# Kernel tuning notes

Measured on AMD Instinct MI355X. Metric: run time of the kernel, lower is better.

The kernel has to match this reference:

```python
import jax, jax.numpy as jnp
import numpy as np

SCALE = 0.125  # 1/sqrt(head_dim=64)

def setup_inputs() -> dict:
    key = jax.random.key(0)
    kq, kk, kv = jax.random.split(key, 3)
    shape = (8, 16, 1024, 64)  # [batch, heads, seq, head_dim]
    q = jax.random.normal(kq, shape, dtype=jnp.float32)
    k = jax.random.normal(kk, shape, dtype=jnp.float32)
    v = jax.random.normal(kv, shape, dtype=jnp.float32)
    return {"q": q, "k": k, "v": v}

def reference(q, k, v):
    # qk = q @ k^T, scaled; softmax over keys; dropout(p=0) is identity; combine with v
    scores = jnp.einsum("bhqd,bhkd->bhqk", q, k) * SCALE
    attn = jax.nn.softmax(scores, axis=-1)
    out = jnp.einsum("bhqk,bhkd->bhqd", attn, v)
    return out
```

## Files before the change

### kernel.cpp

```cpp
#include <hip/hip_runtime.h>
#include <hip/hip_bf16.h>
#include <math.h>

#define SEQ   1024
#define DH    64
#define KBLK  64
#define NBH   128
#define LDK   72
#define C2    0.1803368801111244f
#define DEFER_THR 44.0f

typedef short bf16x8 __attribute__((ext_vector_type(8)));
typedef float f32x4  __attribute__((ext_vector_type(4)));
typedef unsigned u32x4 __attribute__((ext_vector_type(4)));

__device__ inline unsigned short f2bf_rne(float f) {
    union { float f; unsigned u; } x; x.f = f;
    unsigned u = x.u;
    u += 0x7FFFu + ((u >> 16) & 1u);
    return (unsigned short)(u >> 16);
}
__device__ inline unsigned cvt_pk_bf16(float lo, float hi) {
    unsigned r;
    asm("v_cvt_pk_bf16_f32 %0, %1, %2" : "=v"(r) : "v"(lo), "v"(hi));
    return r;
}
__device__ inline void pl32swap(unsigned &a, unsigned &b) {
    asm("v_permlane32_swap_b32 %0, %1" : "+v"(a), "+v"(b));
}
__device__ inline void pl16swap(unsigned &a, unsigned &b) {
    asm("v_permlane16_swap_b32 %0, %1" : "+v"(a), "+v"(b));
}

__device__ inline float wave_red_add(float x) {
    x += __shfl_xor(x, 16);
    x += __shfl_xor(x, 32);
    return x;
}
__device__ inline float wave_red_max(float x) {
    x = fmaxf(x, __shfl_xor(x, 16));
    x = fmaxf(x, __shfl_xor(x, 32));
    return x;
}

__global__ __launch_bounds__(256)
void conv_kv(const float* __restrict__ K, const float* __restrict__ V,
             unsigned short* __restrict__ Kb, unsigned short* __restrict__ Vt) {
    __shared__ unsigned short T[DH][LDK];
    const int kt  = blockIdx.x;
    const int bh  = blockIdx.y;
    const int tid = threadIdx.x;
    const size_t tile = ((size_t)bh * SEQ + kt * KBLK) * DH;

    const float* Ks = K + tile;
    unsigned short* Kd = Kb + tile;
    #pragma unroll
    for (int it = 0; it < 4; ++it) {
        const int e = (it * 256 + tid) * 4;
        float4 f = *(const float4*)(Ks + e);
        union { unsigned short s[4]; uint2 u; } p;
        p.s[0] = f2bf_rne(f.x); p.s[1] = f2bf_rne(f.y);
        p.s[2] = f2bf_rne(f.z); p.s[3] = f2bf_rne(f.w);
        *(uint2*)(Kd + e) = p.u;
    }
    const float* Vs = V + tile;
    #pragma unroll
    for (int it = 0; it < 4; ++it) {
        const int e = (it * 256 + tid) * 4;
        const int kk = e >> 6, d = e & 63;
        float4 f = *(const float4*)(Vs + e);
        T[d + 0][kk] = f2bf_rne(f.x);
        T[d + 1][kk] = f2bf_rne(f.y);
        T[d + 2][kk] = f2bf_rne(f.z);
        T[d + 3][kk] = f2bf_rne(f.w);
    }
    __syncthreads();
    unsigned short* Vd = Vt + tile;
    #pragma unroll
    for (int it = 0; it < 2; ++it) {
        const int e = (it * 256 + tid) * 8;
        const int d = e >> 6, kk0 = e & 63;
        uint4 o = *(const uint4*)&T[d][kk0];
        *(uint4*)(Vd + d * KBLK + kk0) = o;
    }
}

__global__ __launch_bounds__(256)
void attn_fwd(const float* __restrict__ Q,
              const unsigned short* __restrict__ Kb,
              const unsigned short* __restrict__ Vt,
              float* __restrict__ O) {
    __shared__ unsigned short Ksh[2][KBLK][LDK];
    __shared__ unsigned short Vsh[2][DH][LDK];

    const int f  = blockIdx.y * 8 + blockIdx.x;
    const int w  = (f & 7) * 128 + (f >> 3);
    const int qt = w & 7;
    const int bh = w >> 3;

    const int tid  = threadIdx.x;
    const int wave = tid >> 6;
    const int lane = tid & 63;
    const int lhi  = lane >> 4;
    const int llo  = lane & 15;
    const int base = lane & 48;

    const float* Qb = Q + ((size_t)bh * SEQ + qt * 128) * DH;
    float*       Ob = O + ((size_t)bh * SEQ + qt * 128) * DH;

    bf16x8 qfA[2], qfB[2];
    #pragma unroll
    for (int s = 0; s < 2; ++s) {
        const float* pa = Qb + (wave * 32 + llo) * DH + s * 32 + lhi * 8;
        const float* pb = pa + 16 * DH;
        float4 a0 = *(const float4*)(pa), a1 = *(const float4*)(pa + 4);
        float4 b0 = *(const float4*)(pb), b1 = *(const float4*)(pb + 4);
        qfA[s][0]=(short)f2bf_rne(a0.x); qfA[s][1]=(short)f2bf_rne(a0.y);
        qfA[s][2]=(short)f2bf_rne(a0.z); qfA[s][3]=(short)f2bf_rne(a0.w);
        qfA[s][4]=(short)f2bf_rne(a1.x); qfA[s][5]=(short)f2bf_rne(a1.y);
        qfA[s][6]=(short)f2bf_rne(a1.z); qfA[s][7]=(short)f2bf_rne(a1.w);
        qfB[s][0]=(short)f2bf_rne(b0.x); qfB[s][1]=(short)f2bf_rne(b0.y);
        qfB[s][2]=(short)f2bf_rne(b0.z); qfB[s][3]=(short)f2bf_rne(b0.w);
        qfB[s][4]=(short)f2bf_rne(b1.x); qfB[s][5]=(short)f2bf_rne(b1.y);
        qfB[s][6]=(short)f2bf_rne(b1.z); qfB[s][7]=(short)f2bf_rne(b1.w);
    }

    const unsigned short* KbB = Kb + (size_t)bh * SEQ * DH;
    const unsigned short* VtB = Vt + (size_t)bh * SEQ * DH;
    const int soff = tid * 8;
    const int srow = tid >> 3;
    const int scol = (tid & 7) * 8;

    uint4 k0r = *(const uint4*)(KbB + soff);
    uint4 k1r = *(const uint4*)(KbB + 2048 + soff);
    uint4 v0r = *(const uint4*)(VtB + soff);
    uint4 v1r = *(const uint4*)(VtB + 2048 + soff);
    *(uint4*)&Ksh[0][srow][scol]      = k0r;
    *(uint4*)&Ksh[0][32 + srow][scol] = k1r;
    *(uint4*)&Vsh[0][srow][scol]      = v0r;
    *(uint4*)&Vsh[0][32 + srow][scol] = v1r;
    __syncthreads();

    f32x4 accA[4] = {}, accB[4] = {};
    float lA = 0.0f, lB = 0.0f;
    float mCA = 0.0f, mCB = 0.0f;

    for (int kt = 0; kt < SEQ / KBLK; ++kt) {
        const int cur = kt & 1;

        if (kt < 15) {
            const unsigned short* Kt = KbB + (kt + 1) * (KBLK * DH);
            const unsigned short* Vp = VtB + (kt + 1) * (KBLK * DH);
            k0r = *(const uint4*)(Kt + soff);
            k1r = *(const uint4*)(Kt + 2048 + soff);
            v0r = *(const uint4*)(Vp + soff);
            v1r = *(const uint4*)(Vp + 2048 + soff);
        }

        f32x4 stA[4] = {}, stB[4] = {};
        __builtin_amdgcn_s_setprio(1);
        #pragma unroll
        for (int t = 0; t < 4; ++t) {
            bf16x8 k0 = *(const bf16x8*)&Ksh[cur][t * 16 + llo][lhi * 8];
            bf16x8 k1 = *(const bf16x8*)&Ksh[cur][t * 16 + llo][32 + lhi * 8];
            stA[t] = __builtin_amdgcn_mfma_f32_16x16x32_bf16(k0, qfA[0], stA[t], 0, 0, 0);
            stA[t] = __builtin_amdgcn_mfma_f32_16x16x32_bf16(k1, qfA[1], stA[t], 0, 0, 0);
            stB[t] = __builtin_amdgcn_mfma_f32_16x16x32_bf16(k0, qfB[0], stB[t], 0, 0, 0);
            stB[t] = __builtin_amdgcn_mfma_f32_16x16x32_bf16(k1, qfB[1], stB[t], 0, 0, 0);
        }
        __builtin_amdgcn_s_setprio(0);

        if (kt == 0) {
            float ta = stA[0][0], tb = stB[0][0];
            #pragma unroll
            for (int t = 0; t < 4; ++t)
                #pragma unroll
                for (int r = 0; r < 4; ++r) {
                    ta = fmaxf(ta, stA[t][r]);
                    tb = fmaxf(tb, stB[t][r]);
                }
            mCA = wave_red_max(ta) * C2;
            mCB = wave_red_max(tb) * C2;
        }

        float tsA = 0.0f, tsB = 0.0f;
        unsigned wrA[4][2], wrB[4][2];
        #pragma unroll
        for (int t = 0; t < 4; ++t) {
            float a0 = __builtin_amdgcn_exp2f(__builtin_fmaf(stA[t][0], C2, -mCA));
            float a1 = __builtin_amdgcn_exp2f(__builtin_fmaf(stA[t][1], C2, -mCA));
            float a2 = __builtin_amdgcn_exp2f(__builtin_fmaf(stA[t][2], C2, -mCA));
            float a3 = __builtin_amdgcn_exp2f(__builtin_fmaf(stA[t][3], C2, -mCA));
            tsA += (a0 + a1) + (a2 + a3);
            wrA[t][0] = cvt_pk_bf16(a0, a1);
            wrA[t][1] = cvt_pk_bf16(a2, a3);
            float b0 = __builtin_amdgcn_exp2f(__builtin_fmaf(stB[t][0], C2, -mCB));
            float b1 = __builtin_amdgcn_exp2f(__builtin_fmaf(stB[t][1], C2, -mCB));
            float b2 = __builtin_amdgcn_exp2f(__builtin_fmaf(stB[t][2], C2, -mCB));
            float b3 = __builtin_amdgcn_exp2f(__builtin_fmaf(stB[t][3], C2, -mCB));
            tsB += (b0 + b1) + (b2 + b3);
            wrB[t][0] = cvt_pk_bf16(b0, b1);
            wrB[t][1] = cvt_pk_bf16(b2, b3);
        }
        lA += wave_red_add(tsA);
        lB += wave_red_add(tsB);

        unsigned pa0 = wrA[0][0], pb0 = wrA[1][0]; pl32swap(pa0, pb0); pl16swap(pa0, pb0);
        unsigned pa1 = wrA[0][1], pb1 = wrA[1][1]; pl32swap(pa1, pb1); pl16swap(pa1, pb1);
        unsigned pc0 = wrA[2][0], pd0 = wrA[3][0]; pl32swap(pc0, pd0); pl16swap(pc0, pd0);
        unsigned pc1 = wrA[2][1], pd1 = wrA[3][1]; pl32swap(pc1, pd1); pl16swap(pc1, pd1);
        bf16x8 afA0 = __builtin_bit_cast(bf16x8, (u32x4){pa0, pa1, pb0, pb1});
        bf16x8 afA1 = __builtin_bit_cast(bf16x8, (u32x4){pc0, pc1, pd0, pd1});
        unsigned qa0 = wrB[0][0], qb0 = wrB[1][0]; pl32swap(qa0, qb0); pl16swap(qa0, qb0);
        unsigned qa1 = wrB[0][1], qb1 = wrB[1][1]; pl32swap(qa1, qb1); pl16swap(qa1, qb1);
        unsigned qc0 = wrB[2][0], qd0 = wrB[3][0]; pl32swap(qc0, qd0); pl16swap(qc0, qd0);
        unsigned qc1 = wrB[2][1], qd1 = wrB[3][1]; pl32swap(qc1, qd1); pl16swap(qc1, qd1);
        bf16x8 afB0 = __builtin_bit_cast(bf16x8, (u32x4){qa0, qa1, qb0, qb1});
        bf16x8 afB1 = __builtin_bit_cast(bf16x8, (u32x4){qc0, qc1, qd0, qd1});

        __builtin_amdgcn_s_setprio(1);
        #pragma unroll
        for (int dt = 0; dt < 4; ++dt) {
            bf16x8 v0 = *(const bf16x8*)&Vsh[cur][dt * 16 + llo][lhi * 8];
            bf16x8 v1 = *(const bf16x8*)&Vsh[cur][dt * 16 + llo][32 + lhi * 8];
            accA[dt] = __builtin_amdgcn_mfma_f32_16x16x32_bf16(afA0, v0, accA[dt], 0, 0, 0);
            accA[dt] = __builtin_amdgcn_mfma_f32_16x16x32_bf16(afA1, v1, accA[dt], 0, 0, 0);
            accB[dt] = __builtin_amdgcn_mfma_f32_16x16x32_bf16(afB0, v0, accB[dt], 0, 0, 0);
            accB[dt] = __builtin_amdgcn_mfma_f32_16x16x32_bf16(afB1, v1, accB[dt], 0, 0, 0);
        }
        __builtin_amdgcn_s_setprio(0);

        if (kt < 15) {
            const int nxt = cur ^ 1;
            *(uint4*)&Ksh[nxt][srow][scol]      = k0r;
            *(uint4*)&Ksh[nxt][32 + srow][scol] = k1r;
            *(uint4*)&Vsh[nxt][srow][scol]      = v0r;
            *(uint4*)&Vsh[nxt][32 + srow][scol] = v1r;
        }
        __syncthreads();
    }

    const float liA = 1.0f / lA;
    const float liB = 1.0f / lB;
    #pragma unroll
    for (int r = 0; r < 4; ++r) {
        const float la = __shfl(liA, base | (lhi * 4 + r));
        const float lb = __shfl(liB, base | (lhi * 4 + r));
        const int rowA = wave * 32 + lhi * 4 + r;
        #pragma unroll
        for (int dt = 0; dt < 4; ++dt) {
            Ob[rowA * DH + dt * 16 + llo]        = accA[dt][r] * la;
            Ob[(rowA + 16) * DH + dt * 16 + llo] = accB[dt][r] * lb;
        }
    }
}

__global__ __launch_bounds__(256)
void attn_fwd_fb(const float* __restrict__ Q, const float* __restrict__ K,
                 const float* __restrict__ V, float* __restrict__ O) {
    __shared__ unsigned short Ksh[KBLK][LDK];
    __shared__ unsigned short Vsh[DH][LDK];

    const int f  = blockIdx.y * 16 + blockIdx.x;
    const int w  = (f & 7) * 256 + (f >> 3);
    const int qt = w & 15;
    const int bh = w >> 4;

    const int tid  = threadIdx.x;
    const int wave = tid >> 6;
    const int lane = tid & 63;
    const int lhi  = lane >> 4;
    const int llo  = lane & 15;
    const int base = lane & 48;

    const float* Qb = Q + ((size_t)bh * SEQ + qt * 64) * DH;
    float*       Ob = O + ((size_t)bh * SEQ + qt * 64) * DH;

    bf16x8 qf[2];
    #pragma unroll
    for (int s = 0; s < 2; ++s) {
        const float* p = Qb + (wave * 16 + llo) * DH + s * 32 + lhi * 8;
        float4 f0 = *(const float4*)(p), f1 = *(const float4*)(p + 4);
        qf[s][0]=(short)f2bf_rne(f0.x); qf[s][1]=(short)f2bf_rne(f0.y);
        qf[s][2]=(short)f2bf_rne(f0.z); qf[s][3]=(short)f2bf_rne(f0.w);
        qf[s][4]=(short)f2bf_rne(f1.x); qf[s][5]=(short)f2bf_rne(f1.y);
        qf[s][6]=(short)f2bf_rne(f1.z); qf[s][7]=(short)f2bf_rne(f1.w);
    }

    f32x4 acc[4] = {};
    float m_run = -INFINITY, l_run = 0.0f;

    for (int kt = 0; kt < SEQ / KBLK; ++kt) {
        __syncthreads();
        {
            const float* Kt = K + ((size_t)bh * SEQ + kt * KBLK) * DH;
            const float* Vs = V + ((size_t)bh * SEQ + kt * KBLK) * DH;
            #pragma unroll
            for (int it = 0; it < 4; ++it) {
                const int e  = (it * 256 + tid) * 4;
                const int kk = e >> 6, d = e & 63;
                float4 kv = *(const float4*)(Kt + e);
                union { unsigned short s[4]; uint2 u; } pk;
                pk.s[0] = f2bf_rne(kv.x); pk.s[1] = f2bf_rne(kv.y);
                pk.s[2] = f2bf_rne(kv.z); pk.s[3] = f2bf_rne(kv.w);
                *(uint2*)&Ksh[kk][d] = pk.u;
                float4 vv = *(const float4*)(Vs + e);
                Vsh[d + 0][kk] = f2bf_rne(vv.x);
                Vsh[d + 1][kk] = f2bf_rne(vv.y);
                Vsh[d + 2][kk] = f2bf_rne(vv.z);
                Vsh[d + 3][kk] = f2bf_rne(vv.w);
            }
        }
        __syncthreads();

        f32x4 st[4] = {};
        #pragma unroll
        for (int t = 0; t < 4; ++t) {
            bf16x8 k0 = *(const bf16x8*)&Ksh[t * 16 + llo][lhi * 8];
            bf16x8 k1 = *(const bf16x8*)&Ksh[t * 16 + llo][32 + lhi * 8];
            st[t] = __builtin_amdgcn_mfma_f32_16x16x32_bf16(k0, qf[0], st[t], 0, 0, 0);
            st[t] = __builtin_amdgcn_mfma_f32_16x16x32_bf16(k1, qf[1], st[t], 0, 0, 0);
        }

        float tmax = st[0][0];
        #pragma unroll
        for (int t = 0; t < 4; ++t)
            #pragma unroll
            for (int r = 0; r < 4; ++r) tmax = fmaxf(tmax, st[t][r]);
        tmax = wave_red_max(tmax);

        if (__any(tmax > m_run + DEFER_THR)) {
            float mn   = fmaxf(m_run, tmax);
            float corr = exp2f((m_run - mn) * C2);
            m_run = mn;
            l_run *= corr;
            #pragma unroll
            for (int r = 0; r < 4; ++r) {
                float cr = __shfl(corr, base | (lhi * 4 + r));
                #pragma unroll
                for (int dt = 0; dt < 4; ++dt) acc[dt][r] *= cr;
            }
        }

        const float mC = m_run * C2;
        float tsum = 0.0f;
        unsigned wreg[4][2];
        #pragma unroll
        for (int t = 0; t < 4; ++t) {
            float p0 = __builtin_amdgcn_exp2f(__builtin_fmaf(st[t][0], C2, -mC));
            float p1 = __builtin_amdgcn_exp2f(__builtin_fmaf(st[t][1], C2, -mC));
            float p2 = __builtin_amdgcn_exp2f(__builtin_fmaf(st[t][2], C2, -mC));
            float p3 = __builtin_amdgcn_exp2f(__builtin_fmaf(st[t][3], C2, -mC));
            tsum += (p0 + p1) + (p2 + p3);
            wreg[t][0] = cvt_pk_bf16(p0, p1);
            wreg[t][1] = cvt_pk_bf16(p2, p3);
        }
        l_run += wave_red_add(tsum);

        unsigned a0 = wreg[0][0], b0 = wreg[1][0]; pl32swap(a0, b0); pl16swap(a0, b0);
        unsigned a1 = wreg[0][1], b1 = wreg[1][1]; pl32swap(a1, b1); pl16swap(a1, b1);
        unsigned c0 = wreg[2][0], d0 = wreg[3][0]; pl32swap(c0, d0); pl16swap(c0, d0);
        unsigned c1 = wreg[2][1], d1 = wreg[3][1]; pl32swap(c1, d1); pl16swap(c1, d1);
        bf16x8 af0 = __builtin_bit_cast(bf16x8, (u32x4){a0, a1, b0, b1});
        bf16x8 af1 = __builtin_bit_cast(bf16x8, (u32x4){c0, c1, d0, d1});

        #pragma unroll
        for (int dt = 0; dt < 4; ++dt) {
            bf16x8 v0 = *(const bf16x8*)&Vsh[dt * 16 + llo][lhi * 8];
            bf16x8 v1 = *(const bf16x8*)&Vsh[dt * 16 + llo][32 + lhi * 8];
            acc[dt] = __builtin_amdgcn_mfma_f32_16x16x32_bf16(af0, v0, acc[dt], 0, 0, 0);
            acc[dt] = __builtin_amdgcn_mfma_f32_16x16x32_bf16(af1, v1, acc[dt], 0, 0, 0);
        }
    }

    const float linv = 1.0f / l_run;
    #pragma unroll
    for (int r = 0; r < 4; ++r) {
        const float lr = __shfl(linv, base | (lhi * 4 + r));
        const int row = wave * 16 + lhi * 4 + r;
        #pragma unroll
        for (int dt = 0; dt < 4; ++dt)
            Ob[row * DH + dt * 16 + llo] = acc[dt][r] * lr;
    }
}

extern "C" void kernel_launch(void* const* d_in, const int* in_sizes, int n_in,
                              void* d_out, int out_size, void* d_ws, size_t ws_size,
                              hipStream_t stream) {
    const float* q = (const float*)d_in[0];
    const float* k = (const float*)d_in[1];
    const float* v = (const float*)d_in[2];
    float* o = (float*)d_out;

    const size_t nkv = (size_t)NBH * SEQ * DH;
    dim3 block(256);

    if (ws_size >= 2 * nkv * sizeof(unsigned short)) {
        unsigned short* Kb = (unsigned short*)d_ws;
        unsigned short* Vt = Kb + nkv;
        dim3 cgrid(SEQ / KBLK, NBH);
        conv_kv<<<cgrid, block, 0, stream>>>(k, v, Kb, Vt);
        dim3 agrid(SEQ / 128, NBH);
        attn_fwd<<<agrid, block, 0, stream>>>(q, Kb, Vt, o);
    } else {
        dim3 fgrid(SEQ / 64, NBH);
        attn_fwd_fb<<<fgrid, block, 0, stream>>>(q, k, v, o);
    }
}
```

Before: 73.02 us.

## Load V fragments directly to registers and compute row sums via MFMA

V tiles are no longer staged through shared memory; each lane loads its MFMA B-operand fragments straight from global memory into registers, prefetched one tile ahead. The softmax denominator is accumulated with extra MFMAs against a vector of ones instead of wave-wide shuffle reductions, which also removes the final shuffles. Launch bounds request 4 blocks per CU. This cuts LDS traffic and cross-lane reduction work in exchange for more VGPR pressure and uncoalesced-ish global loads for V, plus row sums taken from bf16-rounded probabilities.

```diff
diff --git a/kernel.cpp b/kernel.cpp
--- a/kernel.cpp
+++ b/kernel.cpp
@@ -85,13 +85,12 @@
     }
 }
 
-__global__ __launch_bounds__(256)
+__global__ __launch_bounds__(256, 4)
 void attn_fwd(const float* __restrict__ Q,
               const unsigned short* __restrict__ Kb,
               const unsigned short* __restrict__ Vt,
               float* __restrict__ O) {
     __shared__ unsigned short Ksh[2][KBLK][LDK];
-    __shared__ unsigned short Vsh[2][DH][LDK];
 
     const int f  = blockIdx.y * 8 + blockIdx.x;
     const int w  = (f & 7) * 128 + (f >> 3);
@@ -103,7 +102,6 @@
     const int lane = tid & 63;
     const int lhi  = lane >> 4;
     const int llo  = lane & 15;
-    const int base = lane & 48;
 
     const float* Qb = Q + ((size_t)bh * SEQ + qt * 128) * DH;
     float*       Ob = O + ((size_t)bh * SEQ + qt * 128) * DH;
@@ -125,24 +123,31 @@
         qfB[s][6]=(short)f2bf_rne(b1.z); qfB[s][7]=(short)f2bf_rne(b1.w);
     }
 
+    const bf16x8 ones = {0x3F80, 0x3F80, 0x3F80, 0x3F80,
+                         0x3F80, 0x3F80, 0x3F80, 0x3F80};
+
     const unsigned short* KbB = Kb + (size_t)bh * SEQ * DH;
     const unsigned short* VtB = Vt + (size_t)bh * SEQ * DH;
     const int soff = tid * 8;
     const int srow = tid >> 3;
     const int scol = (tid & 7) * 8;
 
+    const unsigned short* Vl = VtB + llo * KBLK + lhi * 8;
+
     uint4 k0r = *(const uint4*)(KbB + soff);
     uint4 k1r = *(const uint4*)(KbB + 2048 + soff);
-    uint4 v0r = *(const uint4*)(VtB + soff);
-    uint4 v1r = *(const uint4*)(VtB + 2048 + soff);
     *(uint4*)&Ksh[0][srow][scol]      = k0r;
     *(uint4*)&Ksh[0][32 + srow][scol] = k1r;
-    *(uint4*)&Vsh[0][srow][scol]      = v0r;
-    *(uint4*)&Vsh[0][32 + srow][scol] = v1r;
+    bf16x8 vf[4][2];
+    #pragma unroll
+    for (int dt = 0; dt < 4; ++dt) {
+        vf[dt][0] = *(const bf16x8*)(Vl + dt * 16 * KBLK);
+        vf[dt][1] = *(const bf16x8*)(Vl + dt * 16 * KBLK + 32);
+    }
     __syncthreads();
 
     f32x4 accA[4] = {}, accB[4] = {};
-    float lA = 0.0f, lB = 0.0f;
+    f32x4 accLA = {}, accLB = {};
     float mCA = 0.0f, mCB = 0.0f;
 
     for (int kt = 0; kt < SEQ / KBLK; ++kt) {
@@ -150,11 +155,8 @@
 
         if (kt < 15) {
             const unsigned short* Kt = KbB + (kt + 1) * (KBLK * DH);
-            const unsigned short* Vp = VtB + (kt + 1) * (KBLK * DH);
             k0r = *(const uint4*)(Kt + soff);
             k1r = *(const uint4*)(Kt + 2048 + soff);
-            v0r = *(const uint4*)(Vp + soff);
-            v1r = *(const uint4*)(Vp + 2048 + soff);
         }
 
         f32x4 stA[4] = {}, stB[4] = {};
@@ -183,7 +185,6 @@
             mCB = wave_red_max(tb) * C2;
         }
 
-        float tsA = 0.0f, tsB = 0.0f;
         unsigned wrA[4][2], wrB[4][2];
         #pragma unroll
         for (int t = 0; t < 4; ++t) {
@@ -191,19 +192,15 @@
             float a1 = __builtin_amdgcn_exp2f(__builtin_fmaf(stA[t][1], C2, -mCA));
             float a2 = __builtin_amdgcn_exp2f(__builtin_fmaf(stA[t][2], C2, -mCA));
             float a3 = __builtin_amdgcn_exp2f(__builtin_fmaf(stA[t][3], C2, -mCA));
-            tsA += (a0 + a1) + (a2 + a3);
             wrA[t][0] = cvt_pk_bf16(a0, a1);
             wrA[t][1] = cvt_pk_bf16(a2, a3);
             float b0 = __builtin_amdgcn_exp2f(__builtin_fmaf(stB[t][0], C2, -mCB));
             float b1 = __builtin_amdgcn_exp2f(__builtin_fmaf(stB[t][1], C2, -mCB));
             float b2 = __builtin_amdgcn_exp2f(__builtin_fmaf(stB[t][2], C2, -mCB));
             float b3 = __builtin_amdgcn_exp2f(__builtin_fmaf(stB[t][3], C2, -mCB));
-            tsB += (b0 + b1) + (b2 + b3);
             wrB[t][0] = cvt_pk_bf16(b0, b1);
             wrB[t][1] = cvt_pk_bf16(b2, b3);
         }
-        lA += wave_red_add(tsA);
-        lB += wave_red_add(tsB);
 
         unsigned pa0 = wrA[0][0], pb0 = wrA[1][0]; pl32swap(pa0, pb0); pl16swap(pa0, pb0);
         unsigned pa1 = wrA[0][1], pb1 = wrA[1][1]; pl32swap(pa1, pb1); pl16swap(pa1, pb1);
@@ -221,31 +218,38 @@
         __builtin_amdgcn_s_setprio(1);
         #pragma unroll
         for (int dt = 0; dt < 4; ++dt) {
-            bf16x8 v0 = *(const bf16x8*)&Vsh[cur][dt * 16 + llo][lhi * 8];
-            bf16x8 v1 = *(const bf16x8*)&Vsh[cur][dt * 16 + llo][32 + lhi * 8];
-            accA[dt] = __builtin_amdgcn_mfma_f32_16x16x32_bf16(afA0, v0, accA[dt], 0, 0, 0);
-            accA[dt] = __builtin_amdgcn_mfma_f32_16x16x32_bf16(afA1, v1, accA[dt], 0, 0, 0);
-            accB[dt] = __builtin_amdgcn_mfma_f32_16x16x32_bf16(afB0, v0, accB[dt], 0, 0, 0);
-            accB[dt] = __builtin_amdgcn_mfma_f32_16x16x32_bf16(afB1, v1, accB[dt], 0, 0, 0);
-        }
+            accA[dt] = __builtin_amdgcn_mfma_f32_16x16x32_bf16(afA0, vf[dt][0], accA[dt], 0, 0, 0);
+            accA[dt] = __builtin_amdgcn_mfma_f32_16x16x32_bf16(afA1, vf[dt][1], accA[dt], 0, 0, 0);
+            accB[dt] = __builtin_amdgcn_mfma_f32_16x16x32_bf16(afB0, vf[dt][0], accB[dt], 0, 0, 0);
+            accB[dt] = __builtin_amdgcn_mfma_f32_16x16x32_bf16(afB1, vf[dt][1], accB[dt], 0, 0, 0);
+        }
+        accLA = __builtin_amdgcn_mfma_f32_16x16x32_bf16(afA0, ones, accLA, 0, 0, 0);
+        accLA = __builtin_amdgcn_mfma_f32_16x16x32_bf16(afA1, ones, accLA, 0, 0, 0);
+        accLB = __builtin_amdgcn_mfma_f32_16x16x32_bf16(afB0, ones, accLB, 0, 0, 0);
+        accLB = __builtin_amdgcn_mfma_f32_16x16x32_bf16(afB1, ones, accLB, 0, 0, 0);
         __builtin_amdgcn_s_setprio(0);
+
+        if (kt < 15) {
+            const unsigned short* Vp = Vl + (kt + 1) * (KBLK * DH);
+            #pragma unroll
+            for (int dt = 0; dt < 4; ++dt) {
+                vf[dt][0] = *(const bf16x8*)(Vp + dt * 16 * KBLK);
+                vf[dt][1] = *(const bf16x8*)(Vp + dt * 16 * KBLK + 32);
+            }
+        }
 
         if (kt < 15) {
             const int nxt = cur ^ 1;
             *(uint4*)&Ksh[nxt][srow][scol]      = k0r;
             *(uint4*)&Ksh[nxt][32 + srow][scol] = k1r;
-            *(uint4*)&Vsh[nxt][srow][scol]      = v0r;
-            *(uint4*)&Vsh[nxt][32 + srow][scol] = v1r;
         }
         __syncthreads();
     }
 
-    const float liA = 1.0f / lA;
-    const float liB = 1.0f / lB;
     #pragma unroll
     for (int r = 0; r < 4; ++r) {
-        const float la = __shfl(liA, base | (lhi * 4 + r));
-        const float lb = __shfl(liB, base | (lhi * 4 + r));
+        const float la = 1.0f / accLA[r];
+        const float lb = 1.0f / accLB[r];
         const int rowA = wave * 32 + lhi * 4 + r;
         #pragma unroll
         for (int dt = 0; dt < 4; ++dt) {
```

Measured after the change: 137.9 us. +88.9%, slower.
